# Performance work log

Measured on AMD Instinct MI355X. Metric: run time of the kernel, lower is better.

Reference implementation:

```python
import jax, jax.numpy as jnp
import numpy as np

INF = 1e5
EPS = 1e-8
B, NRES, NRIG = 1, 448, 512
C_S, C_Z, C_H, H, PQ, PV = 384, 128, 16, 12, 4, 8


def _quat_to_rot(q):
    q = q / jnp.linalg.norm(q, axis=-1, keepdims=True)
    w, x, y, z = q[..., 0], q[..., 1], q[..., 2], q[..., 3]
    return jnp.stack([
        jnp.stack([1 - 2 * (y * y + z * z), 2 * (x * y - w * z), 2 * (x * z + w * y)], -1),
        jnp.stack([2 * (x * y + w * z), 1 - 2 * (x * x + z * z), 2 * (y * z - w * x)], -1),
        jnp.stack([2 * (x * z - w * y), 2 * (y * z + w * x), 1 - 2 * (x * x + y * y)], -1),
    ], -2)


def setup_inputs() -> dict:
    key = jax.random.key(0)
    ks = jax.random.split(key, 16)
    lin = lambda k, i, o: (jax.random.normal(k, (i, o), jnp.float32) / np.sqrt(i))
    hc = H * C_H
    return dict(
        s=jax.random.normal(ks[0], (B, NRIG, C_S), jnp.float32),
        z=jax.random.normal(ks[1], (B, NRES, NRES, C_Z), jnp.float32),
        rot=_quat_to_rot(jax.random.normal(ks[2], (B, NRIG, 4), jnp.float32)),
        trans=jax.random.normal(ks[3], (B, NRIG, 3), jnp.float32) * 10.0,
        mask=jnp.ones((B, NRIG), jnp.float32),
        rigid_to_res_idx=jax.random.randint(ks[4], (B, NRIG), 0, NRES),
        w_q=lin(ks[5], C_S, hc), b_q=jnp.zeros((hc,), jnp.float32),
        w_kv=lin(ks[6], C_S, 2 * hc), b_kv=jnp.zeros((2 * hc,), jnp.float32),
        w_qp=lin(ks[7], C_S, H * PQ * 3), b_qp=jnp.zeros((H * PQ * 3,), jnp.float32),
        w_kvp=lin(ks[8], C_S, H * (PQ + PV) * 3), b_kvp=jnp.zeros((H * (PQ + PV) * 3,), jnp.float32),
        w_b=lin(ks[9], C_Z, H), b_b=jnp.zeros((H,), jnp.float32),
        w_dz=lin(ks[10], C_Z, C_Z // 4), b_dz=jnp.zeros((C_Z // 4,), jnp.float32),
        head_weights=jnp.full((H,), 0.5413, jnp.float32),  # softplus^-1(1)
        w_out=lin(ks[11], H * (C_Z // 4 + C_H + PV * 4), C_S),
        b_out=jnp.zeros((C_S,), jnp.float32),
    )


def _fwd(s, z, rot, trans, mask, rigid_to_res_idx,
         w_q, b_q, w_kv, b_kv, w_qp, b_qp, w_kvp, b_kvp,
         w_b, b_b, w_dz, b_dz, head_weights, w_out, b_out):
    Bd, nr, _ = s.shape
    nres = z.shape[-2]
    h = w_b.shape[-1]
    ch = w_q.shape[-1] // h
    pq = w_qp.shape[-1] // (3 * h)
    pkv = w_kvp.shape[-1] // (3 * h)
    pv = pkv - pq

    q = (s @ w_q + b_q).reshape(Bd, nr, h, ch)
    kv = (s @ w_kv + b_kv).reshape(Bd, nr, h, 2 * ch)
    k, v = kv[..., :ch], kv[..., ch:]

    def to_pts(flat):
        # flat: [B,nr,3*D] laid out as 3 coordinate chunks -> global-frame pts [B,nr,D,3]
        D = flat.shape[-1] // 3
        p = jnp.moveaxis(flat.reshape(Bd, nr, 3, D), -2, -1)
        return jnp.einsum('bnij,bndj->bndi', rot, p) + trans[:, :, None, :]

    q_pts = to_pts(s @ w_qp + b_qp).reshape(Bd, nr, h, pq, 3)
    kv_pts = to_pts(s @ w_kvp + b_kvp).reshape(Bd, nr, h, pkv, 3)
    k_pts, v_pts = kv_pts[..., :pq, :], kv_pts[..., pq:, :]

    # pair bias gathered rigid->res on both axes
    bi = jnp.arange(Bd)[:, None, None]
    b_pair = z @ w_b + b_b  # [B,Nres,Nres,H]
    b_bcast = b_pair[bi, rigid_to_res_idx[:, :, None], rigid_to_res_idx[:, None, :]]  # [B,nr,nr,H]

    a = jnp.einsum('bihc,bjhc->bhij', q, k) * np.sqrt(1.0 / (3 * ch))
    a = a + np.sqrt(1.0 / 3) * jnp.moveaxis(b_bcast, -1, -3)

    # squared-distance point attention
    diff = q_pts[:, :, None] - k_pts[:, None]  # [B,nr,nr,h,pq,3]
    sq = jnp.sum(diff * diff, -1)              # [B,nr,nr,h,pq]
    hw = jax.nn.softplus(head_weights) * np.sqrt(1.0 / (3 * (pq * 9.0 / 2)))
    pt_att = -0.5 * jnp.sum(sq * hw[:, None], -1)  # [B,nr,nr,h]
    a = a + jnp.moveaxis(pt_att, -1, -3)

    sq_mask = INF * (mask[:, :, None] * mask[:, None, :] - 1.0)
    a = jax.nn.softmax(a + sq_mask[:, None], axis=-1)  # [B,h,nr,nr]

    o = jnp.einsum('bhij,bjhc->bihc', a, v).reshape(Bd, nr, h * ch)

    o_pt_g = jnp.einsum('bhij,bjhpx->bihpx', a, v_pts)  # [B,nr,h,pv,3]
    o_pt = jnp.einsum('bnji,bnhpj->bnhpi', rot, o_pt_g - trans[:, :, None, None, :])  # invert_apply
    o_pt_norm = jnp.sqrt(jnp.sum(o_pt * o_pt, -1) + EPS).reshape(Bd, nr, h * pv)
    o_pt = o_pt.reshape(Bd, nr, h * pv, 3)

    pair_z = z @ w_dz + b_dz  # [B,Nres,Nres,cz4]
    pz_rig = pair_z[jnp.arange(Bd)[:, None], rigid_to_res_idx]  # [B,nr,Nres,cz4]
    # faithful to the torch scatter_add_: the index varies over the QUERY rigid i
    # (constant over keys j), so row i's full softmax mass lands in column res(i).
    onehot = jax.nn.one_hot(rigid_to_res_idx, nres, dtype=a.dtype)  # [B,nr,Nres]
    a_agg = a.sum(-1)[..., None] * onehot[:, None]  # [B,h,nr,Nres]
    o_pair = jnp.einsum('bhin,bind->bihd', a_agg, pz_rig).reshape(Bd, nr, -1)

    feats = jnp.concatenate([o, o_pt[..., 0], o_pt[..., 1], o_pt[..., 2], o_pt_norm, o_pair], -1)
    return feats @ w_out + b_out


def reference(s, z, rot, trans, mask, rigid_to_res_idx, w_q, b_q, w_kv, b_kv, w_qp, b_qp, w_kvp, b_kvp, w_b, b_b, w_dz, b_dz, head_weights, w_out, b_out):
    return _fwd(s, z, rot, trans, mask, rigid_to_res_idx, w_q, b_q, w_kv, b_kv, w_qp, b_qp, w_kvp, b_kvp, w_b, b_b, w_dz, b_dz, head_weights, w_out, b_out)
```

## Files before the change

kernel.cpp:

```cpp
#include <hip/hip_runtime.h>
#include <hip/hip_bf16.h>
#include <math.h>

constexpr int NRIG = 512;
constexpr int NRES = 448;
constexpr int CS   = 384;
constexpr int CZ   = 128;
constexpr int CH   = 16;
constexpr int NH   = 12;
constexpr int PQ   = 4;
constexpr int PV   = 8;
constexpr int HC   = NH * CH;
constexpr int NPAIR = NRES*NRES;
constexpr float INF_ = 100000.0f;

constexpr size_t OFF_Q   = 0;
constexpr size_t OFF_KT  = OFF_Q   + (size_t)NH*NRIG*16;
constexpr size_t OFF_QP  = OFF_KT  + (size_t)NH*16*NRIG;
constexpr size_t OFF_KPT = OFF_QP  + (size_t)NH*NRIG*12;
constexpr size_t OFF_VT  = OFF_KPT + (size_t)NH*12*NRIG;
constexpr size_t OFF_O   = OFF_VT  + (size_t)NH*40*NRIG;
constexpr size_t OFF_OPT = OFF_O   + (size_t)NRIG*HC;
constexpr size_t OFF_RS  = OFF_OPT + (size_t)NRIG*NH*PV*3;
constexpr size_t OFF_BP  = OFF_RS  + (size_t)NRIG*NH;
constexpr size_t OFF_RAW = OFF_BP;
constexpr size_t OFF_F   = OFF_BP;

__global__ __launch_bounds__(256) void proj_gemm_kernel(
    const float* __restrict__ s,
    const float* __restrict__ wq,  const float* __restrict__ bq,
    const float* __restrict__ wkv, const float* __restrict__ bkv,
    const float* __restrict__ wqp, const float* __restrict__ bqp,
    const float* __restrict__ wkvp,const float* __restrict__ bkvp,
    float* __restrict__ ws)
{
    constexpr int BM=64, BN=32, BK=32, LDA=68;
    __shared__ float sA[BK][LDA];
    __shared__ float sB[BK][BN];
    const int m0 = blockIdx.x * BM;
    const int c0 = blockIdx.y * BN;
    const int t  = threadIdx.x;
    const int tx = t & 15, ty = t >> 4;

    float acc[4][2] = {};

    for (int kt = 0; kt < CS/BK; ++kt) {
        const int k0 = kt*BK;
        #pragma unroll
        for (int r = 0; r < 2; ++r) {
            int qd = r*256 + t;
            int m = qd >> 3, kq = (qd & 7) << 2;
            float4 f = *(const float4*)(s + (size_t)(m0+m)*CS + k0 + kq);
            sA[kq+0][m] = f.x; sA[kq+1][m] = f.y;
            sA[kq+2][m] = f.z; sA[kq+3][m] = f.w;
        }
        {
            int kk = t >> 3, c4 = (t & 7) << 2;
            int c = c0 + c4;
            const float* wp; int ld, co;
            if (c < 192)      { wp = wq;   ld = 192; co = c;     }
            else if (c < 576) { wp = wkv;  ld = 384; co = c-192; }
            else if (c < 720) { wp = wqp;  ld = 144; co = c-576; }
            else              { wp = wkvp; ld = 432; co = c-720; }
            float4 f = *(const float4*)(wp + (size_t)(k0+kk)*ld + co);
            *(float4*)&sB[kk][c4] = f;
        }
        __syncthreads();
        #pragma unroll
        for (int kk = 0; kk < BK; ++kk) {
            float4 a = *(const float4*)&sA[kk][ty*4];
            float2 b = *(const float2*)&sB[kk][tx*2];
            acc[0][0] += a.x*b.x; acc[0][1] += a.x*b.y;
            acc[1][0] += a.y*b.x; acc[1][1] += a.y*b.y;
            acc[2][0] += a.z*b.x; acc[2][1] += a.z*b.y;
            acc[3][0] += a.w*b.x; acc[3][1] += a.w*b.y;
        }
        __syncthreads();
    }

    float* qw  = ws + OFF_Q;  float* ktw = ws + OFF_KT;  float* vt = ws + OFF_VT;
    float* raw = ws + OFF_RAW;
    #pragma unroll
    for (int i = 0; i < 4; ++i)
        #pragma unroll
        for (int j = 0; j < 2; ++j) {
            int n = m0 + ty*4 + i;
            int c = c0 + tx*2 + j;
            if (c < 192) {
                int hh = c >> 4, cc = c & 15;
                qw[((size_t)hh*NRIG + n)*16 + cc] = acc[i][j] + bq[c];
            } else if (c < 576) {
                int e = c-192; float val = acc[i][j] + bkv[e];
                int hh = e >> 5, sub = e & 31;
                if (sub < CH) ktw[((size_t)hh*16 + sub)*NRIG + n] = val;
                else          vt [((size_t)hh*40 + (sub-CH))*NRIG + n] = val;
            } else {
                int e = c-576;
                float bb_ = (c < 720) ? bqp[e] : bkvp[c-720];
                raw[(size_t)n*576 + e] = acc[i][j] + bb_;
            }
        }
}

__global__ __launch_bounds__(256) void rotate_kernel(
    const float* __restrict__ rot, const float* __restrict__ trans,
    float* __restrict__ ws)
{
    const int gid = blockIdx.x*256 + threadIdx.x;
    const int n = gid / 192, d = gid % 192;
    const float* raw = ws + OFF_RAW + (size_t)n*576;
    float px, py, pzz;
    if (d < 48) { px = raw[d];      py = raw[48+d];       pzz = raw[96+d]; }
    else { int dd = d-48; px = raw[144+dd]; py = raw[288+dd]; pzz = raw[432+dd]; }
    const float* R = rot   + (size_t)n*9;
    const float* T = trans + (size_t)n*3;
    float gx = R[0]*px + R[1]*py + R[2]*pzz + T[0];
    float gy = R[3]*px + R[4]*py + R[5]*pzz + T[1];
    float gz = R[6]*px + R[7]*py + R[8]*pzz + T[2];
    if (d < 48) {
        int hh = d >> 2, pp = d & 3;
        float* dst = ws + OFF_QP + ((size_t)hh*NRIG + n)*12 + pp*3;
        dst[0]=gx; dst[1]=gy; dst[2]=gz;
    } else {
        int dd = d-48; int hh = dd/12, pp = dd%12;
        if (pp < PQ) {
            float* kpt = ws + OFF_KPT + (size_t)hh*12*NRIG;
            kpt[(size_t)(pp*3+0)*NRIG + n] = gx;
            kpt[(size_t)(pp*3+1)*NRIG + n] = gy;
            kpt[(size_t)(pp*3+2)*NRIG + n] = gz;
        } else {
            float* vt = ws + OFF_VT + ((size_t)hh*40 + 16 + (pp-PQ)*3)*NRIG + n;
            vt[0*NRIG]=gx; vt[1*NRIG]=gy; vt[2*NRIG]=gz;
        }
    }
}

__global__ __launch_bounds__(256) void zwb_kernel(
    const float* __restrict__ z,
    const float* __restrict__ wb, const float* __restrict__ bb,
    float* __restrict__ ws)
{
    constexpr int BR = 64, LDZ = 132;
    __shared__ float sZ[BR][LDZ];
    __shared__ float sW[CZ*12];
    const int t = threadIdx.x;
    const size_t r0 = (size_t)blockIdx.x * BR;

    for (int e = t; e < CZ*12; e += 256) sW[e] = wb[e];
    #pragma unroll
    for (int p = 0; p < 8; ++p) {
        int q = p*256 + t;
        int r = q >> 5, c4 = (q & 31) << 2;
        float4 f = *(const float4*)(z + (r0 + r)*CZ + c4);
        *(float4*)&sZ[r][c4] = f;
    }
    __syncthreads();

    const int r = t >> 2, g = t & 3;
    float a0=0.f, a1=0.f, a2=0.f;
    #pragma unroll 8
    for (int c = 0; c < CZ; ++c) {
        float zv = sZ[r][c];
        const float* w = &sW[c*12 + g*3];
        a0 += zv*w[0]; a1 += zv*w[1]; a2 += zv*w[2];
    }
    const float SC = 0.57735026918962584f;
    float* bp = ws + OFF_BP;
    bp[(size_t)(g*3+0)*NPAIR + r0 + r] = (a0 + bb[g*3+0])*SC;
    bp[(size_t)(g*3+1)*NPAIR + r0 + r] = (a1 + bb[g*3+1])*SC;
    bp[(size_t)(g*3+2)*NPAIR + r0 + r] = (a2 + bb[g*3+2])*SC;
}

__global__ __launch_bounds__(256) void attn_kernel(
    const float* __restrict__ hw_in, const float* __restrict__ mask,
    const int* __restrict__ ridx,
    float* __restrict__ ws)
{
    constexpr int TI = 4;
    const int h    = blockIdx.x;
    const int i0   = blockIdx.y * TI;
    const int t    = threadIdx.x;
    const int lane = t & 63, wid = t >> 6;

    __shared__ float sQ[TI][16];
    __shared__ float sQP[TI][12];
    __shared__ float sE[TI][512];
    __shared__ float redM[TI][4], redS[TI][4];
    __shared__ float sMi[TI];
    __shared__ int   sRi[TI];
    __shared__ float sP[TI][16][44];

    const float* qw  = ws + OFF_Q   + (size_t)h*NRIG*16;
    const float* ktw = ws + OFF_KT  + (size_t)h*16*NRIG;
    const float* qpw = ws + OFF_QP  + (size_t)h*NRIG*12;
    const float* kpt = ws + OFF_KPT + (size_t)h*12*NRIG;
    const float* vt  = ws + OFF_VT  + (size_t)h*40*NRIG;
    const float* bph = ws + OFF_BP  + (size_t)h*NPAIR;

    for (int e = t; e < TI*16; e += 256) sQ[e/16][e%16]  = qw[(size_t)(i0+e/16)*16 + (e%16)];
    for (int e = t; e < TI*12; e += 256) sQP[e/12][e%12] = qpw[(size_t)(i0+e/12)*12 + (e%12)];
    if (t < TI) { sMi[t] = mask[i0+t]; sRi[t] = ridx[i0+t]; }
    __syncthreads();

    const float hwv = -0.5f * log1pf(__expf(hw_in[h])) * 0.13608276348795434f;
    const float QKS = 0.14433756729740643f;

    float lg[2][TI];
    float lmax[TI] = {-1e30f,-1e30f,-1e30f,-1e30f};
    #pragma unroll
    for (int jj = 0; jj < 2; ++jj) {
        int j = t + jj*256;
        float kk[16], kpv[12];
        #pragma unroll
        for (int c = 0; c < 16; ++c) kk[c]  = ktw[(size_t)c*NRIG + j];
        #pragma unroll
        for (int e = 0; e < 12; ++e) kpv[e] = kpt[(size_t)e*NRIG + j];
        float mj = mask[j];
        int rj = ridx[j];
        float bv[TI];
        #pragma unroll
        for (int qq = 0; qq < TI; ++qq)
            bv[qq] = bph[(size_t)sRi[qq]*NRES + rj];
        #pragma unroll
        for (int qq = 0; qq < TI; ++qq) {
            float dot = 0.f;
            #pragma unroll
            for (int c = 0; c < 16; ++c) dot += sQ[qq][c]*kk[c];
            float sq = 0.f;
            #pragma unroll
            for (int e = 0; e < 12; ++e) { float d = sQP[qq][e]-kpv[e]; sq += d*d; }
            float lgt = dot*QKS + bv[qq] + hwv*sq + INF_*(sMi[qq]*mj - 1.0f);
            lg[jj][qq] = lgt;
            lmax[qq] = fmaxf(lmax[qq], lgt);
        }
    }
    #pragma unroll
    for (int sft = 1; sft < 64; sft <<= 1)
        #pragma unroll
        for (int qq=0;qq<TI;++qq) lmax[qq] = fmaxf(lmax[qq], __shfl_xor(lmax[qq], sft));
    if (lane == 0) { for (int qq=0;qq<TI;++qq) redM[qq][wid] = lmax[qq]; }
    __syncthreads();
    float M[TI], psum[TI];
    #pragma unroll
    for (int qq=0;qq<TI;++qq) {
        M[qq] = fmaxf(fmaxf(redM[qq][0],redM[qq][1]),fmaxf(redM[qq][2],redM[qq][3]));
        psum[qq]=0.f;
    }
    #pragma unroll
    for (int jj = 0; jj < 2; ++jj) {
        int j = t + jj*256;
        #pragma unroll
        for (int qq=0;qq<TI;++qq) {
            float e = __expf(lg[jj][qq] - M[qq]);
            sE[qq][j] = e;
            psum[qq] += e;
        }
    }
    #pragma unroll
    for (int sft = 1; sft < 64; sft <<= 1)
        #pragma unroll
        for (int qq=0;qq<TI;++qq) psum[qq] += __shfl_xor(psum[qq], sft);
    if (lane == 0) { for (int qq=0;qq<TI;++qq) redS[qq][wid] = psum[qq]; }
    __syncthreads();

    {
        const int c0 = wid*10;
        float acc[10][TI];
        #pragma unroll
        for (int ci=0;ci<10;++ci)
            #pragma unroll
            for (int qq=0;qq<TI;++qq) acc[ci][qq]=0.f;

        #pragma unroll
        for (int m = 0; m < 8; ++m) {
            const int j = lane + 64*m;
            float ev[TI];
            #pragma unroll
            for (int qq=0;qq<TI;++qq) ev[qq] = sE[qq][j];
            #pragma unroll
            for (int ci = 0; ci < 10; ++ci) {
                float vv = vt[(size_t)(c0+ci)*NRIG + j];
                #pragma unroll
                for (int qq=0;qq<TI;++qq) acc[ci][qq] += ev[qq]*vv;
            }
        }
        #pragma unroll
        for (int ci=0;ci<10;++ci)
            #pragma unroll
            for (int qq=0;qq<TI;++qq) {
                acc[ci][qq] += __shfl_xor(acc[ci][qq], 1);
                acc[ci][qq] += __shfl_xor(acc[ci][qq], 2);
            }
        if ((lane & 3) == 0) {
            const int g = lane >> 2;
            #pragma unroll
            for (int qq=0;qq<TI;++qq)
                #pragma unroll
                for (int ci=0;ci<10;++ci)
                    sP[qq][g][c0+ci] = acc[ci][qq];
        }
    }
    __syncthreads();

    if (t < TI*41) {
        const int qq = t / 41, c = t % 41;
        const int n = i0 + qq;
        float S = redS[qq][0]+redS[qq][1]+redS[qq][2]+redS[qq][3];
        float Sinv = 1.0f / S;
        if (c == 40) {
            (ws + OFF_RS)[(size_t)n*NH + h] = S * Sinv;
        } else {
            float acc = 0.f;
            #pragma unroll
            for (int g = 0; g < 16; ++g) acc += sP[qq][g][c];
            acc *= Sinv;
            if (c < 16) (ws + OFF_O  )[((size_t)n*NH + h)*CH + c]      = acc;
            else        (ws + OFF_OPT)[((size_t)n*NH + h)*24 + (c-16)] = acc;
        }
    }
}

__global__ __launch_bounds__(256) void feats_kernel(
    const float* __restrict__ rot, const float* __restrict__ trans,
    const float* __restrict__ z, const int* __restrict__ ridx,
    const float* __restrict__ wdz, const float* __restrict__ bdz,
    float* __restrict__ ws)
{
    constexpr int TI = 4;
    __shared__ float sZd[TI][CZ];
    __shared__ float sPz[TI][32];
    const int i0 = blockIdx.x*TI;
    const int t  = threadIdx.x;
    float* F = ws + OFF_F;
    const float* o_ws = ws + OFF_O;  const float* optg = ws + OFF_OPT;
    const float* rs   = ws + OFF_RS;

    for (int e = t; e < TI*CZ; e += 256) {
        int qq = e >> 7, c = e & 127;
        int ri = ridx[i0+qq];
        sZd[qq][c] = z[((size_t)ri*NRES + ri)*CZ + c];
    }
    for (int e = t; e < TI*HC; e += 256) {
        int qq = e/HC, c = e%HC;
        F[(size_t)(i0+qq)*960 + c] = o_ws[(size_t)(i0+qq)*HC + c];
    }
    for (int e = t; e < TI*96; e += 256) {
        int qq = e/96, hp = e%96; int n = i0+qq;
        const float* g = optg + ((size_t)n*NH + hp/PV)*24 + (hp%PV)*3;
        float gx = g[0]-trans[n*3+0], gy = g[1]-trans[n*3+1], gz = g[2]-trans[n*3+2];
        const float* R = rot + (size_t)n*9;
        float lx = R[0]*gx + R[3]*gy + R[6]*gz;
        float ly = R[1]*gx + R[4]*gy + R[7]*gz;
        float lz = R[2]*gx + R[5]*gy + R[8]*gz;
        float* Fr = F + (size_t)n*960;
        Fr[192+hp] = lx; Fr[288+hp] = ly; Fr[384+hp] = lz;
        Fr[480+hp] = sqrtf(lx*lx+ly*ly+lz*lz + 1e-8f);
    }
    __syncthreads();
    if (t < TI*32) {
        int qq = t >> 5, d = t & 31;
        float acc = 0.f;
        #pragma unroll 8
        for (int c = 0; c < CZ; ++c) acc += sZd[qq][c] * wdz[(size_t)c*32 + d];
        sPz[qq][d] = acc + bdz[d];
    }
    __syncthreads();
    for (int e = t; e < TI*384; e += 256) {
        int qq = e/384, hd = e%384; int n = i0+qq;
        F[(size_t)n*960 + 576 + hd] = rs[(size_t)n*NH + (hd>>5)] * sPz[qq][hd&31];
    }
}

__global__ __launch_bounds__(256) void out_gemm_kernel(
    const float* __restrict__ w_out, const float* __restrict__ b_out,
    const float* __restrict__ ws, float* __restrict__ out)
{
    constexpr int BM=64, BN=32, BK=32, LDA=68;
    __shared__ float sA[BK][LDA];
    __shared__ float sB[BK][BN];
    const float* F = ws + OFF_F;
    const int m0 = blockIdx.x * BM;
    const int c0 = blockIdx.y * BN;
    const int t  = threadIdx.x;
    const int tx = t & 15, ty = t >> 4;

    float acc[4][2] = {};

    for (int kt = 0; kt < 960/BK; ++kt) {
        const int k0 = kt*BK;
        #pragma unroll
        for (int r = 0; r < 2; ++r) {
            int qd = r*256 + t;
            int m = qd >> 3, kq = (qd & 7) << 2;
            float4 f = *(const float4*)(F + (size_t)(m0+m)*960 + k0 + kq);
            sA[kq+0][m] = f.x; sA[kq+1][m] = f.y;
            sA[kq+2][m] = f.z; sA[kq+3][m] = f.w;
        }
        {
            int kk = t >> 3, c4 = (t & 7) << 2;
            float4 f = *(const float4*)(w_out + (size_t)(k0+kk)*CS + c0 + c4);
            *(float4*)&sB[kk][c4] = f;
        }
        __syncthreads();
        #pragma unroll
        for (int kk = 0; kk < BK; ++kk) {
            float4 a = *(const float4*)&sA[kk][ty*4];
            float2 b = *(const float2*)&sB[kk][tx*2];
            acc[0][0] += a.x*b.x; acc[0][1] += a.x*b.y;
            acc[1][0] += a.y*b.x; acc[1][1] += a.y*b.y;
            acc[2][0] += a.z*b.x; acc[2][1] += a.z*b.y;
            acc[3][0] += a.w*b.x; acc[3][1] += a.w*b.y;
        }
        __syncthreads();
    }

    #pragma unroll
    for (int i = 0; i < 4; ++i)
        #pragma unroll
        for (int j = 0; j < 2; ++j) {
            int n = m0 + ty*4 + i;
            int c = c0 + tx*2 + j;
            out[(size_t)n*CS + c] = acc[i][j] + b_out[c];
        }
}

extern "C" void kernel_launch(void* const* d_in, const int* in_sizes, int n_in,
                              void* d_out, int out_size, void* d_ws, size_t ws_size,
                              hipStream_t stream)
{
    const float* s     = (const float*)d_in[0];
    const float* z     = (const float*)d_in[1];
    const float* rot   = (const float*)d_in[2];
    const float* trans = (const float*)d_in[3];
    const float* mask  = (const float*)d_in[4];
    const int*   ridx  = (const int*)  d_in[5];
    const float* wq    = (const float*)d_in[6];
    const float* bq    = (const float*)d_in[7];
    const float* wkv   = (const float*)d_in[8];
    const float* bkv   = (const float*)d_in[9];
    const float* wqp   = (const float*)d_in[10];
    const float* bqp   = (const float*)d_in[11];
    const float* wkvp  = (const float*)d_in[12];
    const float* bkvp  = (const float*)d_in[13];
    const float* wb    = (const float*)d_in[14];
    const float* bb    = (const float*)d_in[15];
    const float* wdz   = (const float*)d_in[16];
    const float* bdz   = (const float*)d_in[17];
    const float* hw    = (const float*)d_in[18];
    const float* wout  = (const float*)d_in[19];
    const float* bout  = (const float*)d_in[20];
    float* ws  = (float*)d_ws;
    float* out = (float*)d_out;

    hipLaunchKernelGGL(proj_gemm_kernel, dim3(NRIG/64, 1152/32), dim3(256), 0, stream,
        s, wq,bq, wkv,bkv, wqp,bqp, wkvp,bkvp, ws);
    hipLaunchKernelGGL(rotate_kernel, dim3(NRIG*192/256), dim3(256), 0, stream,
        rot, trans, ws);
    hipLaunchKernelGGL(zwb_kernel, dim3(NPAIR/64), dim3(256), 0, stream,
        z, wb, bb, ws);
    hipLaunchKernelGGL(attn_kernel, dim3(NH, NRIG/4), dim3(256), 0, stream,
        hw, mask, ridx, ws);
    hipLaunchKernelGGL(feats_kernel, dim3(NRIG/4), dim3(256), 0, stream,
        rot, trans, z, ridx, wdz, bdz, ws);
    hipLaunchKernelGGL(out_gemm_kernel, dim3(NRIG/64, CS/32), dim3(256), 0, stream,
        wout, bout, ws, out);
}
```

Before: 127.3 us.

## Fuse projection and pair-bias kernels, single-pass softmax, split-K output GEMM

Merges the z·w_b pair-bias kernel and the projection GEMM into one launch with block-index dispatch, using a swizzled shared layout and 2-way channel split for the bias part. The attention kernel drops the running-max pass and computes the softmax denominator as an extra ones channel in the PV accumulation, processing 8 query rows per block. The output GEMM is split along K into three partial products summed by a new reduce kernel. Removing max subtraction reduces passes and syncs but risks exp overflow for large logits; split-K adds a workspace round trip.

```diff
diff --git a/kernel.cpp b/kernel.cpp
--- a/kernel.cpp
+++ b/kernel.cpp
@@ -13,6 +13,7 @@
 constexpr int HC   = NH * CH;
 constexpr int NPAIR = NRES*NRES;
 constexpr float INF_ = 100000.0f;
+constexpr float SC_ = 0.57735026918962584f;
 
 constexpr size_t OFF_Q   = 0;
 constexpr size_t OFF_KT  = OFF_Q   + (size_t)NH*NRIG*16;
@@ -23,10 +24,14 @@
 constexpr size_t OFF_OPT = OFF_O   + (size_t)NRIG*HC;
 constexpr size_t OFF_RS  = OFF_OPT + (size_t)NRIG*NH*PV*3;
 constexpr size_t OFF_BP  = OFF_RS  + (size_t)NRIG*NH;
-constexpr size_t OFF_RAW = OFF_BP;
-constexpr size_t OFF_F   = OFF_BP;
-
-__global__ __launch_bounds__(256) void proj_gemm_kernel(
+constexpr size_t OFF_RAW = OFF_BP  + (size_t)NH*NPAIR;
+constexpr size_t OFF_F   = OFF_RAW + (size_t)NRIG*576;
+constexpr size_t OFF_P3  = OFF_F   + (size_t)NRIG*960;
+
+constexpr int ZWB_BLOCKS = NPAIR/128;
+
+__global__ __launch_bounds__(256) void prep_kernel(
+    const float* __restrict__ z,  const float* __restrict__ wb, const float* __restrict__ bb,
     const float* __restrict__ s,
     const float* __restrict__ wq,  const float* __restrict__ bq,
     const float* __restrict__ wkv, const float* __restrict__ bkv,
@@ -34,81 +39,127 @@
     const float* __restrict__ wkvp,const float* __restrict__ bkvp,
     float* __restrict__ ws)
 {
-    constexpr int BM=64, BN=32, BK=32, LDA=68;
-    __shared__ float sA[BK][LDA];
-    __shared__ float sB[BK][BN];
-    const int m0 = blockIdx.x * BM;
-    const int c0 = blockIdx.y * BN;
-    const int t  = threadIdx.x;
-    const int tx = t & 15, ty = t >> 4;
-
-    float acc[4][2] = {};
-
-    for (int kt = 0; kt < CS/BK; ++kt) {
-        const int k0 = kt*BK;
-        #pragma unroll
-        for (int r = 0; r < 2; ++r) {
-            int qd = r*256 + t;
-            int m = qd >> 3, kq = (qd & 7) << 2;
-            float4 f = *(const float4*)(s + (size_t)(m0+m)*CS + k0 + kq);
-            sA[kq+0][m] = f.x; sA[kq+1][m] = f.y;
-            sA[kq+2][m] = f.z; sA[kq+3][m] = f.w;
-        }
-        {
-            int kk = t >> 3, c4 = (t & 7) << 2;
-            int c = c0 + c4;
-            const float* wp; int ld, co;
-            if (c < 192)      { wp = wq;   ld = 192; co = c;     }
-            else if (c < 576) { wp = wkv;  ld = 384; co = c-192; }
-            else if (c < 720) { wp = wqp;  ld = 144; co = c-576; }
-            else              { wp = wkvp; ld = 432; co = c-720; }
-            float4 f = *(const float4*)(wp + (size_t)(k0+kk)*ld + co);
-            *(float4*)&sB[kk][c4] = f;
+    __shared__ float smem[18560];
+    const int t = threadIdx.x;
+
+    if ((int)blockIdx.x < ZWB_BLOCKS) {
+        float* sZ   = smem;
+        float* sRed = smem + 16896;
+        const size_t r0 = (size_t)blockIdx.x * 128;
+        #pragma unroll
+        for (int k = 0; k < 16; ++k) {
+            int i = k*256 + t;
+            int row = i >> 5, c4 = i & 31;
+            float4 f = *(const float4*)(z + (r0+row)*CZ + (c4<<2));
+            *(float4*)&sZ[row*132 + ((c4 ^ (row&7))<<2)] = f;
         }
         __syncthreads();
-        #pragma unroll
-        for (int kk = 0; kk < BK; ++kk) {
-            float4 a = *(const float4*)&sA[kk][ty*4];
-            float2 b = *(const float2*)&sB[kk][tx*2];
-            acc[0][0] += a.x*b.x; acc[0][1] += a.x*b.y;
-            acc[1][0] += a.y*b.x; acc[1][1] += a.y*b.y;
-            acc[2][0] += a.z*b.x; acc[2][1] += a.z*b.y;
-            acc[3][0] += a.w*b.x; acc[3][1] += a.w*b.y;
+        const int wid = t >> 6, lane = t & 63;
+        const int rB = ((wid>>1)<<6) | lane;
+        const int ch = wid & 1;
+        float acc[12] = {0,0,0,0,0,0,0,0,0,0,0,0};
+        const int cb = ch*16;
+        #pragma unroll
+        for (int i = 0; i < 16; ++i) {
+            const int c4 = cb + i;
+            float4 zf = *(const float4*)&sZ[rB*132 + ((c4 ^ (rB&7))<<2)];
+            #pragma unroll
+            for (int e = 0; e < 4; ++e) {
+                const float zv = (&zf.x)[e];
+                const float* wr = wb + (c4*4+e)*12;
+                #pragma unroll
+                for (int h = 0; h < 12; ++h) acc[h] += zv * wr[h];
+            }
+        }
+        if (ch == 0) {
+            #pragma unroll
+            for (int h = 0; h < 12; ++h) sRed[rB*13 + h] = acc[h];
         }
         __syncthreads();
-    }
-
-    float* qw  = ws + OFF_Q;  float* ktw = ws + OFF_KT;  float* vt = ws + OFF_VT;
-    float* raw = ws + OFF_RAW;
-    #pragma unroll
-    for (int i = 0; i < 4; ++i)
-        #pragma unroll
-        for (int j = 0; j < 2; ++j) {
-            int n = m0 + ty*4 + i;
-            int c = c0 + tx*2 + j;
-            if (c < 192) {
-                int hh = c >> 4, cc = c & 15;
-                qw[((size_t)hh*NRIG + n)*16 + cc] = acc[i][j] + bq[c];
-            } else if (c < 576) {
-                int e = c-192; float val = acc[i][j] + bkv[e];
-                int hh = e >> 5, sub = e & 31;
-                if (sub < CH) ktw[((size_t)hh*16 + sub)*NRIG + n] = val;
-                else          vt [((size_t)hh*40 + (sub-CH))*NRIG + n] = val;
-            } else {
-                int e = c-576;
-                float bb_ = (c < 720) ? bqp[e] : bkvp[c-720];
-                raw[(size_t)n*576 + e] = acc[i][j] + bb_;
-            }
-        }
+        if (ch == 1) {
+            float* bp = ws + OFF_BP;
+            #pragma unroll
+            for (int h = 0; h < 12; ++h) {
+                float v = (acc[h] + sRed[rB*13 + h] + bb[h]) * SC_;
+                bp[(size_t)h*NPAIR + r0 + rB] = v;
+            }
+        }
+    } else {
+        constexpr int BM=64, BN=32, BK=32, LDA=68;
+        float (*sA)[LDA] = (float(*)[LDA])smem;
+        float (*sB)[BN]  = (float(*)[BN])(smem + 2176);
+        const int bid = (int)blockIdx.x - ZWB_BLOCKS;
+        const int m0 = (bid & 7) * BM;
+        const int c0 = (bid >> 3) * BN;
+        const int tx = t & 15, ty = t >> 4;
+
+        float acc[4][2] = {};
+        for (int kt = 0; kt < CS/BK; ++kt) {
+            const int k0 = kt*BK;
+            #pragma unroll
+            for (int r = 0; r < 2; ++r) {
+                int qd = r*256 + t;
+                int m = qd >> 3, kq = (qd & 7) << 2;
+                float4 f = *(const float4*)(s + (size_t)(m0+m)*CS + k0 + kq);
+                sA[kq+0][m] = f.x; sA[kq+1][m] = f.y;
+                sA[kq+2][m] = f.z; sA[kq+3][m] = f.w;
+            }
+            {
+                int kk = t >> 3, c4 = (t & 7) << 2;
+                int c = c0 + c4;
+                const float* wp; int ld, co;
+                if (c < 192)      { wp = wq;   ld = 192; co = c;     }
+                else if (c < 576) { wp = wkv;  ld = 384; co = c-192; }
+                else if (c < 720) { wp = wqp;  ld = 144; co = c-576; }
+                else              { wp = wkvp; ld = 432; co = c-720; }
+                float4 f = *(const float4*)(wp + (size_t)(k0+kk)*ld + co);
+                *(float4*)&sB[kk][c4] = f;
+            }
+            __syncthreads();
+            #pragma unroll
+            for (int kk = 0; kk < BK; ++kk) {
+                float4 a = *(const float4*)&sA[kk][ty*4];
+                float2 b = *(const float2*)&sB[kk][tx*2];
+                acc[0][0] += a.x*b.x; acc[0][1] += a.x*b.y;
+                acc[1][0] += a.y*b.x; acc[1][1] += a.y*b.y;
+                acc[2][0] += a.z*b.x; acc[2][1] += a.z*b.y;
+                acc[3][0] += a.w*b.x; acc[3][1] += a.w*b.y;
+            }
+            __syncthreads();
+        }
+        float* qw  = ws + OFF_Q;  float* ktw = ws + OFF_KT;  float* vt = ws + OFF_VT;
+        float* raw = ws + OFF_RAW;
+        #pragma unroll
+        for (int i = 0; i < 4; ++i)
+            #pragma unroll
+            for (int j = 0; j < 2; ++j) {
+                int n = m0 + ty*4 + i;
+                int c = c0 + tx*2 + j;
+                if (c < 192) {
+                    int hh = c >> 4, cc = c & 15;
+                    qw[((size_t)hh*NRIG + n)*16 + cc] = acc[i][j] + bq[c];
+                } else if (c < 576) {
+                    int e = c-192; float val = acc[i][j] + bkv[e];
+                    int hh = e >> 5, sub = e & 31;
+                    if (sub < CH) ktw[((size_t)hh*16 + sub)*NRIG + n] = val;
+                    else          vt [((size_t)hh*40 + (sub-CH))*NRIG + n] = val;
+                } else {
+                    int e = c-576;
+                    float bb_ = (c < 720) ? bqp[e] : bkvp[c-720];
+                    raw[(size_t)n*576 + e] = acc[i][j] + bb_;
+                }
+            }
+    }
 }
 
 __global__ __launch_bounds__(256) void rotate_kernel(
     const float* __restrict__ rot, const float* __restrict__ trans,
-    float* __restrict__ ws)
+    const float* __restrict__ raw_in, float* __restrict__ qpw,
+    float* __restrict__ kptw, float* __restrict__ vtw)
 {
     const int gid = blockIdx.x*256 + threadIdx.x;
     const int n = gid / 192, d = gid % 192;
-    const float* raw = ws + OFF_RAW + (size_t)n*576;
+    const float* raw = raw_in + (size_t)n*576;
     float px, py, pzz;
     if (d < 48) { px = raw[d];      py = raw[48+d];       pzz = raw[96+d]; }
     else { int dd = d-48; px = raw[144+dd]; py = raw[288+dd]; pzz = raw[432+dd]; }
@@ -119,204 +170,141 @@
     float gz = R[6]*px + R[7]*py + R[8]*pzz + T[2];
     if (d < 48) {
         int hh = d >> 2, pp = d & 3;
-        float* dst = ws + OFF_QP + ((size_t)hh*NRIG + n)*12 + pp*3;
+        float* dst = qpw + ((size_t)hh*NRIG + n)*12 + pp*3;
         dst[0]=gx; dst[1]=gy; dst[2]=gz;
     } else {
         int dd = d-48; int hh = dd/12, pp = dd%12;
         if (pp < PQ) {
-            float* kpt = ws + OFF_KPT + (size_t)hh*12*NRIG;
+            float* kpt = kptw + (size_t)hh*12*NRIG;
             kpt[(size_t)(pp*3+0)*NRIG + n] = gx;
             kpt[(size_t)(pp*3+1)*NRIG + n] = gy;
             kpt[(size_t)(pp*3+2)*NRIG + n] = gz;
         } else {
-            float* vt = ws + OFF_VT + ((size_t)hh*40 + 16 + (pp-PQ)*3)*NRIG + n;
+            float* vt = vtw + ((size_t)hh*40 + 16 + (pp-PQ)*3)*NRIG + n;
             vt[0*NRIG]=gx; vt[1*NRIG]=gy; vt[2*NRIG]=gz;
         }
     }
-}
-
-__global__ __launch_bounds__(256) void zwb_kernel(
-    const float* __restrict__ z,
-    const float* __restrict__ wb, const float* __restrict__ bb,
-    float* __restrict__ ws)
-{
-    constexpr int BR = 64, LDZ = 132;
-    __shared__ float sZ[BR][LDZ];
-    __shared__ float sW[CZ*12];
-    const int t = threadIdx.x;
-    const size_t r0 = (size_t)blockIdx.x * BR;
-
-    for (int e = t; e < CZ*12; e += 256) sW[e] = wb[e];
-    #pragma unroll
-    for (int p = 0; p < 8; ++p) {
-        int q = p*256 + t;
-        int r = q >> 5, c4 = (q & 31) << 2;
-        float4 f = *(const float4*)(z + (r0 + r)*CZ + c4);
-        *(float4*)&sZ[r][c4] = f;
-    }
-    __syncthreads();
-
-    const int r = t >> 2, g = t & 3;
-    float a0=0.f, a1=0.f, a2=0.f;
-    #pragma unroll 8
-    for (int c = 0; c < CZ; ++c) {
-        float zv = sZ[r][c];
-        const float* w = &sW[c*12 + g*3];
-        a0 += zv*w[0]; a1 += zv*w[1]; a2 += zv*w[2];
-    }
-    const float SC = 0.57735026918962584f;
-    float* bp = ws + OFF_BP;
-    bp[(size_t)(g*3+0)*NPAIR + r0 + r] = (a0 + bb[g*3+0])*SC;
-    bp[(size_t)(g*3+1)*NPAIR + r0 + r] = (a1 + bb[g*3+1])*SC;
-    bp[(size_t)(g*3+2)*NPAIR + r0 + r] = (a2 + bb[g*3+2])*SC;
 }
 
 __global__ __launch_bounds__(256) void attn_kernel(
     const float* __restrict__ hw_in, const float* __restrict__ mask,
     const int* __restrict__ ridx,
-    float* __restrict__ ws)
-{
-    constexpr int TI = 4;
+    const float* __restrict__ qw_all,  const float* __restrict__ ktw_all,
+    const float* __restrict__ qpw_all, const float* __restrict__ kpt_all,
+    const float* __restrict__ vt_all,  const float* __restrict__ bp_all,
+    float* __restrict__ o_out, float* __restrict__ opt_out, float* __restrict__ rs_out)
+{
+    constexpr int TI = 8;
     const int h    = blockIdx.x;
     const int i0   = blockIdx.y * TI;
     const int t    = threadIdx.x;
     const int lane = t & 63, wid = t >> 6;
 
-    __shared__ float sQ[TI][16];
-    __shared__ float sQP[TI][12];
-    __shared__ float sE[TI][512];
-    __shared__ float redM[TI][4], redS[TI][4];
-    __shared__ float sMi[TI];
-    __shared__ int   sRi[TI];
-    __shared__ float sP[TI][16][44];
-
-    const float* qw  = ws + OFF_Q   + (size_t)h*NRIG*16;
-    const float* ktw = ws + OFF_KT  + (size_t)h*16*NRIG;
-    const float* qpw = ws + OFF_QP  + (size_t)h*NRIG*12;
-    const float* kpt = ws + OFF_KPT + (size_t)h*12*NRIG;
-    const float* vt  = ws + OFF_VT  + (size_t)h*40*NRIG;
-    const float* bph = ws + OFF_BP  + (size_t)h*NPAIR;
-
-    for (int e = t; e < TI*16; e += 256) sQ[e/16][e%16]  = qw[(size_t)(i0+e/16)*16 + (e%16)];
-    for (int e = t; e < TI*12; e += 256) sQP[e/12][e%12] = qpw[(size_t)(i0+e/12)*12 + (e%12)];
-    if (t < TI) { sMi[t] = mask[i0+t]; sRi[t] = ridx[i0+t]; }
-    __syncthreads();
+    __shared__ float sE[TI*516];
+    __shared__ float sP[16][TI][45];
+    __shared__ float sS[TI];
+
+    const float* qw  = qw_all  + (size_t)h*NRIG*16;
+    const float* ktw = ktw_all + (size_t)h*16*NRIG;
+    const float* qpw = qpw_all + (size_t)h*NRIG*12;
+    const float* kpt = kpt_all + (size_t)h*12*NRIG;
+    const float* vt  = vt_all  + (size_t)h*40*NRIG;
+    const float* bph = bp_all  + (size_t)h*NPAIR;
 
     const float hwv = -0.5f * log1pf(__expf(hw_in[h])) * 0.13608276348795434f;
     const float QKS = 0.14433756729740643f;
 
-    float lg[2][TI];
-    float lmax[TI] = {-1e30f,-1e30f,-1e30f,-1e30f};
     #pragma unroll
     for (int jj = 0; jj < 2; ++jj) {
-        int j = t + jj*256;
+        const int j = t + jj*256;
         float kk[16], kpv[12];
         #pragma unroll
-        for (int c = 0; c < 16; ++c) kk[c]  = ktw[(size_t)c*NRIG + j];
-        #pragma unroll
-        for (int e = 0; e < 12; ++e) kpv[e] = kpt[(size_t)e*NRIG + j];
-        float mj = mask[j];
-        int rj = ridx[j];
-        float bv[TI];
-        #pragma unroll
-        for (int qq = 0; qq < TI; ++qq)
-            bv[qq] = bph[(size_t)sRi[qq]*NRES + rj];
+        for (int c = 0; c < 16; ++c) kk[c]  = ktw[c*NRIG + j];
+        #pragma unroll
+        for (int e = 0; e < 12; ++e) kpv[e] = kpt[e*NRIG + j];
+        const float mj = mask[j];
+        const int   rj = ridx[j];
         #pragma unroll
         for (int qq = 0; qq < TI; ++qq) {
+            const float* qv  = qw  + (size_t)(i0+qq)*16;
+            const float* qpv = qpw + (size_t)(i0+qq)*12;
+            const float  mi  = mask[i0+qq];
+            const int    ri  = ridx[i0+qq];
             float dot = 0.f;
             #pragma unroll
-            for (int c = 0; c < 16; ++c) dot += sQ[qq][c]*kk[c];
+            for (int c = 0; c < 16; ++c) dot += qv[c]*kk[c];
             float sq = 0.f;
             #pragma unroll
-            for (int e = 0; e < 12; ++e) { float d = sQP[qq][e]-kpv[e]; sq += d*d; }
-            float lgt = dot*QKS + bv[qq] + hwv*sq + INF_*(sMi[qq]*mj - 1.0f);
-            lg[jj][qq] = lgt;
-            lmax[qq] = fmaxf(lmax[qq], lgt);
-        }
-    }
-    #pragma unroll
-    for (int sft = 1; sft < 64; sft <<= 1)
-        #pragma unroll
-        for (int qq=0;qq<TI;++qq) lmax[qq] = fmaxf(lmax[qq], __shfl_xor(lmax[qq], sft));
-    if (lane == 0) { for (int qq=0;qq<TI;++qq) redM[qq][wid] = lmax[qq]; }
+            for (int e = 0; e < 12; ++e) { float d = qpv[e]-kpv[e]; sq += d*d; }
+            const float bv = bph[(size_t)ri*NRES + rj];
+            const float lgt = dot*QKS + bv + hwv*sq + INF_*(mi*mj - 1.0f);
+            sE[qq*516 + j] = __expf(lgt);
+        }
+    }
     __syncthreads();
-    float M[TI], psum[TI];
-    #pragma unroll
-    for (int qq=0;qq<TI;++qq) {
-        M[qq] = fmaxf(fmaxf(redM[qq][0],redM[qq][1]),fmaxf(redM[qq][2],redM[qq][3]));
-        psum[qq]=0.f;
-    }
-    #pragma unroll
-    for (int jj = 0; jj < 2; ++jj) {
-        int j = t + jj*256;
-        #pragma unroll
-        for (int qq=0;qq<TI;++qq) {
-            float e = __expf(lg[jj][qq] - M[qq]);
-            sE[qq][j] = e;
-            psum[qq] += e;
-        }
-    }
-    #pragma unroll
-    for (int sft = 1; sft < 64; sft <<= 1)
-        #pragma unroll
-        for (int qq=0;qq<TI;++qq) psum[qq] += __shfl_xor(psum[qq], sft);
-    if (lane == 0) { for (int qq=0;qq<TI;++qq) redS[qq][wid] = psum[qq]; }
-    __syncthreads();
 
     {
-        const int c0 = wid*10;
-        float acc[10][TI];
-        #pragma unroll
-        for (int ci=0;ci<10;++ci)
+        float acc[11][TI];
+        #pragma unroll
+        for (int ci=0;ci<11;++ci)
             #pragma unroll
             for (int qq=0;qq<TI;++qq) acc[ci][qq]=0.f;
 
         #pragma unroll
         for (int m = 0; m < 8; ++m) {
-            const int j = lane + 64*m;
+            const int j = lane + (m<<6);
             float ev[TI];
             #pragma unroll
-            for (int qq=0;qq<TI;++qq) ev[qq] = sE[qq][j];
-            #pragma unroll
-            for (int ci = 0; ci < 10; ++ci) {
-                float vv = vt[(size_t)(c0+ci)*NRIG + j];
+            for (int qq=0;qq<TI;++qq) ev[qq] = sE[qq*516 + j];
+            #pragma unroll
+            for (int ci = 0; ci < 11; ++ci) {
+                if (ci < 10 || wid == 0) {
+                    const int c = wid + (ci<<2);
+                    const float vv = (c == 40) ? 1.0f : vt[(size_t)c*NRIG + j];
+                    #pragma unroll
+                    for (int qq=0;qq<TI;++qq) acc[ci][qq] += ev[qq]*vv;
+                }
+            }
+        }
+        #pragma unroll
+        for (int ci=0;ci<11;++ci)
+            if (ci < 10 || wid == 0)
                 #pragma unroll
-                for (int qq=0;qq<TI;++qq) acc[ci][qq] += ev[qq]*vv;
-            }
-        }
-        #pragma unroll
-        for (int ci=0;ci<10;++ci)
-            #pragma unroll
-            for (int qq=0;qq<TI;++qq) {
-                acc[ci][qq] += __shfl_xor(acc[ci][qq], 1);
-                acc[ci][qq] += __shfl_xor(acc[ci][qq], 2);
-            }
+                for (int qq=0;qq<TI;++qq) {
+                    acc[ci][qq] += __shfl_xor(acc[ci][qq], 1);
+                    acc[ci][qq] += __shfl_xor(acc[ci][qq], 2);
+                }
         if ((lane & 3) == 0) {
             const int g = lane >> 2;
             #pragma unroll
-            for (int qq=0;qq<TI;++qq)
-                #pragma unroll
-                for (int ci=0;ci<10;++ci)
-                    sP[qq][g][c0+ci] = acc[ci][qq];
+            for (int ci=0;ci<11;++ci)
+                if (ci < 10 || wid == 0) {
+                    const int c = wid + (ci<<2);
+                    #pragma unroll
+                    for (int qq=0;qq<TI;++qq) sP[g][qq][c] = acc[ci][qq];
+                }
         }
     }
     __syncthreads();
 
-    if (t < TI*41) {
-        const int qq = t / 41, c = t % 41;
+    if (t < TI) {
+        float S = 0.f;
+        #pragma unroll
+        for (int g = 0; g < 16; ++g) S += sP[g][t][40];
+        sS[t] = S;
+    }
+    __syncthreads();
+
+    for (int e = t; e < TI*41; e += 256) {
+        const int qq = e / 41, c = e % 41;
         const int n = i0 + qq;
-        float S = redS[qq][0]+redS[qq][1]+redS[qq][2]+redS[qq][3];
-        float Sinv = 1.0f / S;
-        if (c == 40) {
-            (ws + OFF_RS)[(size_t)n*NH + h] = S * Sinv;
-        } else {
-            float acc = 0.f;
-            #pragma unroll
-            for (int g = 0; g < 16; ++g) acc += sP[qq][g][c];
-            acc *= Sinv;
-            if (c < 16) (ws + OFF_O  )[((size_t)n*NH + h)*CH + c]      = acc;
-            else        (ws + OFF_OPT)[((size_t)n*NH + h)*24 + (c-16)] = acc;
-        }
+        float sum = 0.f;
+        #pragma unroll
+        for (int g = 0; g < 16; ++g) sum += sP[g][qq][c];
+        const float val = sum * (1.0f / sS[qq]);
+        if (c < 16)       o_out[((size_t)n*NH + h)*CH + c]        = val;
+        else if (c < 40)  opt_out[((size_t)n*NH + h)*24 + (c-16)] = val;
+        else              rs_out[(size_t)n*NH + h]                = val;
     }
 }
 
@@ -324,16 +312,14 @@
     const float* __restrict__ rot, const float* __restrict__ trans,
     const float* __restrict__ z, const int* __restrict__ ridx,
     const float* __restrict__ wdz, const float* __restrict__ bdz,
-    float* __restrict__ ws)
+    const float* __restrict__ o_ws, const float* __restrict__ optg,
+    const float* __restrict__ rs, float* __restrict__ F)
 {
     constexpr int TI = 4;
     __shared__ float sZd[TI][CZ];
     __shared__ float sPz[TI][32];
     const int i0 = blockIdx.x*TI;
     const int t  = threadIdx.x;
-    float* F = ws + OFF_F;
-    const float* o_ws = ws + OFF_O;  const float* optg = ws + OFF_OPT;
-    const float* rs   = ws + OFF_RS;
 
     for (int e = t; e < TI*CZ; e += 256) {
         int qq = e >> 7, c = e & 127;
@@ -372,22 +358,21 @@
 }
 
 __global__ __launch_bounds__(256) void out_gemm_kernel(
-    const float* __restrict__ w_out, const float* __restrict__ b_out,
-    const float* __restrict__ ws, float* __restrict__ out)
+    const float* __restrict__ w_out, const float* __restrict__ F,
+    float* __restrict__ P)
 {
     constexpr int BM=64, BN=32, BK=32, LDA=68;
     __shared__ float sA[BK][LDA];
     __shared__ float sB[BK][BN];
-    const float* F = ws + OFF_F;
     const int m0 = blockIdx.x * BM;
     const int c0 = blockIdx.y * BN;
+    const int ks = blockIdx.z;
     const int t  = threadIdx.x;
     const int tx = t & 15, ty = t >> 4;
 
     float acc[4][2] = {};
-
-    for (int kt = 0; kt < 960/BK; ++kt) {
-        const int k0 = kt*BK;
+    for (int kt = 0; kt < 10; ++kt) {
+        const int k0 = ks*320 + kt*BK;
         #pragma unroll
         for (int r = 0; r < 2; ++r) {
             int qd = r*256 + t;
@@ -413,15 +398,31 @@
         }
         __syncthreads();
     }
-
     #pragma unroll
     for (int i = 0; i < 4; ++i)
         #pragma unroll
         for (int j = 0; j < 2; ++j) {
             int n = m0 + ty*4 + i;
             int c = c0 + tx*2 + j;
-            out[(size_t)n*CS + c] = acc[i][j] + b_out[c];
-        }
+            P[(size_t)ks*NRIG*CS + (size_t)n*CS + c] = acc[i][j];
+        }
+}
+
+__global__ __launch_bounds__(256) void reduce_kernel(
+    const float* __restrict__ P, const float* __restrict__ b_out,
+    float* __restrict__ out)
+{
+    const int i4 = blockIdx.x*256 + threadIdx.x;
+    const size_t base = (size_t)i4 * 4;
+    float4 a = *(const float4*)(P + base);
+    float4 b = *(const float4*)(P + (size_t)NRIG*CS + base);
+    float4 c = *(const float4*)(P + (size_t)2*NRIG*CS + base);
+    const int cc = (int)(base % CS);
+    float4 bv = *(const float4*)(b_out + cc);
+    float4 r;
+    r.x = a.x+b.x+c.x+bv.x; r.y = a.y+b.y+c.y+bv.y;
+    r.z = a.z+b.z+c.z+bv.z; r.w = a.w+b.w+c.w+bv.w;
+    *(float4*)(out + base) = r;
 }
 
 extern "C" void kernel_launch(void* const* d_in, const int* in_sizes, int n_in,
@@ -452,16 +453,17 @@
     float* ws  = (float*)d_ws;
     float* out = (float*)d_out;
 
-    hipLaunchKernelGGL(proj_gemm_kernel, dim3(NRIG/64, 1152/32), dim3(256), 0, stream,
-        s, wq,bq, wkv,bkv, wqp,bqp, wkvp,bkvp, ws);
+    hipLaunchKernelGGL(prep_kernel, dim3(ZWB_BLOCKS + 288), dim3(256), 0, stream,
+        z, wb, bb, s, wq,bq, wkv,bkv, wqp,bqp, wkvp,bkvp, ws);
     hipLaunchKernelGGL(rotate_kernel, dim3(NRIG*192/256), dim3(256), 0, stream,
-        rot, trans, ws);
-    hipLaunchKernelGGL(zwb_kernel, dim3(NPAIR/64), dim3(256), 0, stream,
-        z, wb, bb, ws);
-    hipLaunchKernelGGL(attn_kernel, dim3(NH, NRIG/4), dim3(256), 0, stream,
-        hw, mask, ridx, ws);
+        rot, trans, ws+OFF_RAW, ws+OFF_QP, ws+OFF_KPT, ws+OFF_VT);
+    hipLaunchKernelGGL(attn_kernel, dim3(NH, NRIG/8), dim3(256), 0, stream,
+        hw, mask, ridx, ws+OFF_Q, ws+OFF_KT, ws+OFF_QP, ws+OFF_KPT,
+        ws+OFF_VT, ws+OFF_BP, ws+OFF_O, ws+OFF_OPT, ws+OFF_RS);
     hipLaunchKernelGGL(feats_kernel, dim3(NRIG/4), dim3(256), 0, stream,
-        rot, trans, z, ridx, wdz, bdz, ws);
-    hipLaunchKernelGGL(out_gemm_kernel, dim3(NRIG/64, CS/32), dim3(256), 0, stream,
-        wout, bout, ws, out);
-}
+        rot, trans, z, ridx, wdz, bdz, ws+OFF_O, ws+OFF_OPT, ws+OFF_RS, ws+OFF_F);
+    hipLaunchKernelGGL(out_gemm_kernel, dim3(NRIG/64, CS/32, 3), dim3(256), 0, stream,
+        wout, ws+OFF_F, ws+OFF_P3);
+    hipLaunchKernelGGL(reduce_kernel, dim3(NRIG*CS/4/256), dim3(256), 0, stream,
+        ws+OFF_P3, bout, out);
+}
```

Result: no change. 125.2 us, median of 5 (-1.6%).
